# Optimization experiments

Hardware: AMD Instinct MI355X
Metric: run time of the kernel (lower is better)

## Reference

```python
import jax, jax.numpy as jnp
import numpy as np

HIDDEN = 512
INPUT = 512
BATCH = 16384


def _quant_dequant(w):
    # mirrors torch: scale = max(|w|)/127 + 1e-8; int8 round-clamp; dequantize
    scale = jnp.max(jnp.abs(w)) / 127.0 + 1e-8
    q = jnp.clip(jnp.round(w / scale), -128, 127)
    return q * scale


def setup_inputs() -> dict:
    key = jax.random.key(0)
    ks = jax.random.split(key, 7)
    x = jax.random.normal(ks[0], (BATCH, INPUT), dtype=jnp.float32)
    h_prev = jax.random.normal(ks[1], (BATCH, HIDDEN), dtype=jnp.float32)
    c_prev = jax.random.normal(ks[2], (BATCH, HIDDEN), dtype=jnp.float32)
    w_ih = _quant_dequant(jax.random.normal(ks[3], (4 * HIDDEN, INPUT), dtype=jnp.float32) * 0.05)
    w_hh = _quant_dequant(jax.random.normal(ks[4], (4 * HIDDEN, HIDDEN), dtype=jnp.float32) * 0.05)
    bias_ih = jax.random.normal(ks[5], (4 * HIDDEN,), dtype=jnp.float32) * 0.05
    bias_hh = jax.random.normal(ks[6], (4 * HIDDEN,), dtype=jnp.float32) * 0.05
    return {"x": x, "h_prev": h_prev, "c_prev": c_prev,
            "w_ih": w_ih, "w_hh": w_hh, "bias_ih": bias_ih, "bias_hh": bias_hh}


def reference(x, h_prev, c_prev, w_ih, w_hh, bias_ih, bias_hh):
    # gates: [B, 4H]
    gates = x @ w_ih.T + bias_ih + h_prev @ w_hh.T + bias_hh
    i_g, f_g, g_g, o_g = jnp.split(gates, 4, axis=1)
    i_g = jax.nn.sigmoid(i_g)
    f_g = jax.nn.sigmoid(f_g)
    g_g = jnp.tanh(g_g)
    o_g = jax.nn.sigmoid(o_g)
    c_new = f_g * c_prev + i_g * g_g
    h_new = o_g * jnp.tanh(c_new)
    return (h_new, c_new)
```

## Files before the change

### kernel.cpp

```cpp
#include <hip/hip_runtime.h>


typedef __attribute__((ext_vector_type(4))) int int4v;
typedef __attribute__((ext_vector_type(8))) short short8;
typedef __attribute__((ext_vector_type(4))) float f32x4;
typedef unsigned int u32;
typedef unsigned short u16;
typedef unsigned char u8;

#define BATCH 16384
#define HID 512
#define KTOT 1024
#define BM 256
#define KSTEPS 8
#define TILEA_BYTES 32768
#define TILEW_BYTES 16384
#define NBM 64
#define NBN 16
#define WSA_BYTES ((size_t)NBM * KSTEPS * TILEA_BYTES)
#define WSW_BYTES ((size_t)NBN * KSTEPS * TILEW_BYTES)
#define SCALE_OFF (WSA_BYTES + WSW_BYTES)
#define PART_OFF (SCALE_OFF + 65536)
#define SW_OFF (PART_OFF + 2048)
#define WS_NEEDED (SW_OFF + 64)

__device__ __forceinline__ float sigmoidf_(float v) { return 1.0f / (1.0f + __expf(-v)); }
__device__ __forceinline__ float tanhf_(float v) { return 1.0f - 2.0f / (__expf(2.0f * v) + 1.0f); }

__device__ __forceinline__ void gload_lds16(const void* g, void* l) {
    __builtin_amdgcn_global_load_lds(
        (const __attribute__((address_space(1))) u32*)g,
        (__attribute__((address_space(3))) u32*)l, 16, 0, 0);
}

__device__ __forceinline__ u32 pack4(float a, float b, float c, float d, float inv) {
    int q0 = (int)rintf(a * inv), q1 = (int)rintf(b * inv);
    int q2 = (int)rintf(c * inv), q3 = (int)rintf(d * inv);
    return (q0 & 255) | ((q1 & 255) << 8) | ((q2 & 255) << 16) | ((q3 & 255) << 24);
}

__global__ __launch_bounds__(256) void wmax_part(
    const float* __restrict__ w_ih, const float* __restrict__ w_hh, float* __restrict__ part)
{
    const u32 b = blockIdx.x;
    const float* src = (b < 256) ? (w_ih + (size_t)b * 4096) : (w_hh + (size_t)(b - 256) * 4096);
    const u32 t = threadIdx.x;
    float am = 0.f;
    const float4* p = (const float4*)src + t;
    #pragma unroll
    for (int j = 0; j < 4; ++j) {
        float4 v = p[j * 256];
        am = fmaxf(am, fmaxf(fmaxf(fabsf(v.x), fabsf(v.y)), fmaxf(fabsf(v.z), fabsf(v.w))));
    }
    #pragma unroll
    for (int o = 32; o >= 1; o >>= 1) am = fmaxf(am, __shfl_xor(am, o, 64));
    __shared__ float red[4];
    if ((t & 63) == 0) red[t >> 6] = am;
    __syncthreads();
    if (t == 0) part[b] = fmaxf(fmaxf(red[0], red[1]), fmaxf(red[2], red[3]));
}

__global__ __launch_bounds__(256) void pack_w(
    const float* __restrict__ w_ih, const float* __restrict__ w_hh,
    const float* __restrict__ part, u8* __restrict__ wsW, float* __restrict__ swOut)
{
    const u32 t = threadIdx.x;
    float am = fmaxf(part[t], part[t + 256]);
    #pragma unroll
    for (int o = 32; o >= 1; o >>= 1) am = fmaxf(am, __shfl_xor(am, o, 64));
    __shared__ float red[4];
    if ((t & 63) == 0) red[t >> 6] = am;
    __syncthreads();
    const float wmax = fmaxf(fmaxf(red[0], red[1]), fmaxf(red[2], red[3]));
    const float inv = 127.0f / wmax;
    if (blockIdx.x == 0 && t == 0) *swOut = wmax * (1.0f / 127.0f);

    const u32 widx = blockIdx.x * 256 + t;
    const u32 cphys = widx & 7;
    const u32 row = (widx >> 3) & 127;
    const u32 ks = (widx >> 10) & 7;
    const u32 bn = widx >> 13;
    const u32 clog = cphys ^ (row & 7);
    const u32 g = row >> 5, rr = row & 31;
    const u32 wrow = g * 512 + bn * 32 + rr;
    const u32 kglob = ks * 128 + clog * 16;
    const float* src = (kglob < 512) ? (w_ih + (size_t)wrow * 512 + kglob)
                                     : (w_hh + (size_t)wrow * 512 + (kglob - 512));
    u32 wds[4];
    #pragma unroll
    for (int j = 0; j < 4; ++j) {
        float4 v = *((const float4*)src + j);
        wds[j] = pack4(v.x, v.y, v.z, v.w, inv);
    }
    int4v val = {(int)wds[0], (int)wds[1], (int)wds[2], (int)wds[3]};
    *(int4v*)(wsW + (size_t)widx * 16) = val;
}

__global__ __launch_bounds__(256) void pack_a(
    const float* __restrict__ x, const float* __restrict__ h_prev,
    u8* __restrict__ wsA, float* __restrict__ aScale)
{
    const u32 t = threadIdx.x;
    const u32 lane = t & 63;
    const u32 m = blockIdx.x * 4 + (t >> 6);
    const u32 k0 = lane * 16;
    const float* src = (k0 < 512) ? (x + (size_t)m * 512 + k0)
                                  : (h_prev + (size_t)m * 512 + (k0 - 512));
    float4 v[4];
    #pragma unroll
    for (int j = 0; j < 4; ++j) v[j] = *((const float4*)src + j);
    float am = 0.f;
    #pragma unroll
    for (int j = 0; j < 4; ++j)
        am = fmaxf(am, fmaxf(fmaxf(fabsf(v[j].x), fabsf(v[j].y)),
                             fmaxf(fabsf(v[j].z), fabsf(v[j].w))));
    #pragma unroll
    for (int o = 32; o >= 1; o >>= 1) am = fmaxf(am, __shfl_xor(am, o, 64));
    const float inv = (am > 0.f) ? 127.0f / am : 0.f;
    if (lane == 0) aScale[m] = am * (1.0f / 127.0f);
    u32 wds[4];
    #pragma unroll
    for (int j = 0; j < 4; ++j) wds[j] = pack4(v[j].x, v[j].y, v[j].z, v[j].w, inv);
    const u32 bm = m >> 8, row = m & 255;
    const u32 ks = lane >> 3, clog = lane & 7;
    const u32 cphys = clog ^ (row & 7);
    int4v val = {(int)wds[0], (int)wds[1], (int)wds[2], (int)wds[3]};
    *(int4v*)(wsA + ((((size_t)bm * 8 + ks) * 256 + row) * 8 + cphys) * 16) = val;
}

__global__ __launch_bounds__(256, 2) void lstm_gemm(
    const u8* __restrict__ wsA, const u8* __restrict__ wsW,
    const float* __restrict__ aScale, const float* __restrict__ swPtr,
    const float* __restrict__ c_prev,
    const float* __restrict__ b_ih, const float* __restrict__ b_hh,
    float* __restrict__ h_out, float* __restrict__ c_out)
{
    __shared__ u8 sA[TILEA_BYTES];
    __shared__ u8 sW[TILEW_BYTES];

    const int t = threadIdx.x;
    const int bn = blockIdx.x & 15;
    const int bm = blockIdx.x >> 4;
    const int n0 = bn * 32;
    const int rowBase = bm * BM;

    const int lane = t & 63;
    const int wv = t >> 6;
    const int colin = lane & 15;
    const int quad = lane >> 4;
    const int stageOff = t * 16;

    int4v acc[4][2][4];
    #pragma unroll
    for (int rf = 0; rf < 4; ++rf)
        #pragma unroll
        for (int cc = 0; cc < 2; ++cc)
            #pragma unroll
            for (int g = 0; g < 4; ++g)
                acc[rf][cc][g] = (int4v){0, 0, 0, 0};

    const char* gA = (const char*)wsA + (size_t)bm * KSTEPS * TILEA_BYTES;
    const char* gW = (const char*)wsW + (size_t)bn * KSTEPS * TILEW_BYTES;

    #pragma unroll 1
    for (int ks = 0; ks < KSTEPS; ++ks) {
        __syncthreads();
        #pragma unroll
        for (int j = 0; j < 8; ++j)
            gload_lds16(gA + (size_t)ks * TILEA_BYTES + j * 4096 + stageOff,
                        (char*)sA + j * 4096 + stageOff);
        #pragma unroll
        for (int j = 0; j < 4; ++j)
            gload_lds16(gW + (size_t)ks * TILEW_BYTES + j * 4096 + stageOff,
                        (char*)sW + j * 4096 + stageOff);
        __syncthreads();

        #pragma unroll
        for (int ks2 = 0; ks2 < 2; ++ks2) {
            int4v af[4];
            #pragma unroll
            for (int rf = 0; rf < 4; ++rf) {
                const int row = wv * 64 + rf * 16 + colin;
                const int boff = row * 128 + (((ks2 * 4 + quad) ^ (row & 7)) * 16);
                af[rf] = *(const int4v*)((const char*)sA + boff);
            }
            int4v bfr[2][4];
            #pragma unroll
            for (int cc = 0; cc < 2; ++cc)
                #pragma unroll
                for (int g = 0; g < 4; ++g) {
                    const int wrow = g * 32 + cc * 16 + colin;
                    const int boff = wrow * 128 + (((ks2 * 4 + quad) ^ (wrow & 7)) * 16);
                    bfr[cc][g] = *(const int4v*)((const char*)sW + boff);
                }
            #pragma unroll
            for (int rf = 0; rf < 4; ++rf)
                #pragma unroll
                for (int cc = 0; cc < 2; ++cc)
                    #pragma unroll
                    for (int g = 0; g < 4; ++g)
                        acc[rf][cc][g] = __builtin_amdgcn_mfma_i32_16x16x64_i8(
                            af[rf], bfr[cc][g], acc[rf][cc][g], 0, 0, 0);
        }
    }

    const float sw = *swPtr;
    float rsc[4][4];
    #pragma unroll
    for (int rf = 0; rf < 4; ++rf)
        #pragma unroll
        for (int reg = 0; reg < 4; ++reg)
            rsc[rf][reg] = aScale[rowBase + wv * 64 + rf * 16 + quad * 4 + reg] * sw;

    float bsum[2][4];
    #pragma unroll
    for (int cc = 0; cc < 2; ++cc) {
        const int colg = n0 + cc * 16 + colin;
        #pragma unroll
        for (int g = 0; g < 4; ++g)
            bsum[cc][g] = b_ih[g * 512 + colg] + b_hh[g * 512 + colg];
    }

    #pragma unroll
    for (int rf = 0; rf < 4; ++rf)
        #pragma unroll
        for (int cc = 0; cc < 2; ++cc) {
            const int colg = n0 + cc * 16 + colin;
            #pragma unroll
            for (int reg = 0; reg < 4; ++reg) {
                const int row = rowBase + wv * 64 + rf * 16 + quad * 4 + reg;
                const size_t off = (size_t)row * 512 + colg;
                const float s = rsc[rf][reg];
                const float ig = (float)acc[rf][cc][0][reg] * s + bsum[cc][0];
                const float fg = (float)acc[rf][cc][1][reg] * s + bsum[cc][1];
                const float gg = (float)acc[rf][cc][2][reg] * s + bsum[cc][2];
                const float og = (float)acc[rf][cc][3][reg] * s + bsum[cc][3];
                const float cp = __builtin_nontemporal_load(c_prev + off);
                const float cn = sigmoidf_(fg) * cp + sigmoidf_(ig) * tanhf_(gg);
                const float hn = sigmoidf_(og) * tanhf_(cn);
                __builtin_nontemporal_store(hn, h_out + off);
                __builtin_nontemporal_store(cn, c_out + off);
            }
        }
}

#define LDSK 72
__device__ __forceinline__ u16 f2bf(float f) {
    u32 u = __builtin_bit_cast(u32, f);
    u += 0x7FFFu + ((u >> 16) & 1u);
    return (u16)(u >> 16);
}
__global__ __launch_bounds__(256, 3) void lstm_fused_v1(
    const float* __restrict__ x, const float* __restrict__ h_prev,
    const float* __restrict__ c_prev, const float* __restrict__ w_ih,
    const float* __restrict__ w_hh, const float* __restrict__ b_ih,
    const float* __restrict__ b_hh, float* __restrict__ h_out,
    float* __restrict__ c_out)
{
    __shared__ u16 sA[128][LDSK];
    __shared__ u16 sW[128][LDSK];
    const int t = threadIdx.x;
    const int bn = blockIdx.x & 15, bm = blockIdx.x >> 4;
    const int n0 = bn * 32, rowBase = bm * 128;
    const int srow = t >> 4, scol = t & 15;
    const int lane = t & 63, wv = t >> 6, colin = lane & 15, quad = lane >> 4;
    f32x4 acc[2][2][4];
    #pragma unroll
    for (int rf = 0; rf < 2; ++rf)
        #pragma unroll
        for (int cc = 0; cc < 2; ++cc)
            #pragma unroll
            for (int g = 0; g < 4; ++g) acc[rf][cc][g] = (f32x4){0.f, 0.f, 0.f, 0.f};
    for (int k0 = 0; k0 < KTOT; k0 += 64) {
        const int kk = (k0 < 512) ? k0 : (k0 - 512);
        const float* aSrc = (k0 < 512) ? x : h_prev;
        const float* wSrc = (k0 < 512) ? w_ih : w_hh;
        __syncthreads();
        #pragma unroll
        for (int p = 0; p < 8; ++p) {
            const int r = srow + p * 16;
            const float4 av = *(const float4*)(aSrc + (size_t)(rowBase + r) * 512 + kk + scol * 4);
            ushort4 ap; ap.x = f2bf(av.x); ap.y = f2bf(av.y); ap.z = f2bf(av.z); ap.w = f2bf(av.w);
            *(ushort4*)&sA[r][scol * 4] = ap;
            const int gate = r >> 5, rr = r & 31;
            const float4 wvv = *(const float4*)(wSrc + (size_t)(gate * 512 + n0 + rr) * 512 + kk + scol * 4);
            ushort4 wp; wp.x = f2bf(wvv.x); wp.y = f2bf(wvv.y); wp.z = f2bf(wvv.z); wp.w = f2bf(wvv.w);
            *(ushort4*)&sW[r][scol * 4] = wp;
        }
        __syncthreads();
        #pragma unroll
        for (int ks = 0; ks < 2; ++ks) {
            short8 af[2];
            #pragma unroll
            for (int rf = 0; rf < 2; ++rf)
                af[rf] = *(const short8*)&sA[wv * 32 + rf * 16 + colin][ks * 32 + quad * 8];
            short8 bfr[2][4];
            #pragma unroll
            for (int cc = 0; cc < 2; ++cc)
                #pragma unroll
                for (int g = 0; g < 4; ++g)
                    bfr[cc][g] = *(const short8*)&sW[g * 32 + cc * 16 + colin][ks * 32 + quad * 8];
            #pragma unroll
            for (int rf = 0; rf < 2; ++rf)
                #pragma unroll
                for (int cc = 0; cc < 2; ++cc)
                    #pragma unroll
                    for (int g = 0; g < 4; ++g)
                        acc[rf][cc][g] = __builtin_amdgcn_mfma_f32_16x16x32_bf16(
                            af[rf], bfr[cc][g], acc[rf][cc][g], 0, 0, 0);
        }
    }
    float bsum[2][4];
    #pragma unroll
    for (int cc = 0; cc < 2; ++cc) {
        const int colg = n0 + cc * 16 + colin;
        #pragma unroll
        for (int g = 0; g < 4; ++g) bsum[cc][g] = b_ih[g * 512 + colg] + b_hh[g * 512 + colg];
    }
    #pragma unroll
    for (int rf = 0; rf < 2; ++rf)
        #pragma unroll
        for (int cc = 0; cc < 2; ++cc) {
            const int colg = n0 + cc * 16 + colin;
            #pragma unroll
            for (int reg = 0; reg < 4; ++reg) {
                const int row = rowBase + wv * 32 + rf * 16 + quad * 4 + reg;
                const size_t off = (size_t)row * 512 + colg;
                const float ig = acc[rf][cc][0][reg] + bsum[cc][0];
                const float fg = acc[rf][cc][1][reg] + bsum[cc][1];
                const float gg = acc[rf][cc][2][reg] + bsum[cc][2];
                const float og = acc[rf][cc][3][reg] + bsum[cc][3];
                const float cp = c_prev[off];
                const float cn = sigmoidf_(fg) * cp + sigmoidf_(ig) * tanhf_(gg);
                const float hn = sigmoidf_(og) * tanhf_(cn);
                h_out[off] = hn;
                c_out[off] = cn;
            }
        }
}

extern "C" void kernel_launch(void* const* d_in, const int* in_sizes, int n_in,
                              void* d_out, int out_size, void* d_ws, size_t ws_size,
                              hipStream_t stream) {
    const float* x      = (const float*)d_in[0];
    const float* h_prev = (const float*)d_in[1];
    const float* c_prev = (const float*)d_in[2];
    const float* w_ih   = (const float*)d_in[3];
    const float* w_hh   = (const float*)d_in[4];
    const float* b_ih   = (const float*)d_in[5];
    const float* b_hh   = (const float*)d_in[6];
    float* h_out = (float*)d_out;
    float* c_out = h_out + (size_t)BATCH * HID;

    if (ws_size >= WS_NEEDED) {
        u8* wsA = (u8*)d_ws;
        u8* wsW = (u8*)d_ws + WSA_BYTES;
        float* aScale = (float*)((char*)d_ws + SCALE_OFF);
        float* part   = (float*)((char*)d_ws + PART_OFF);
        float* swOut  = (float*)((char*)d_ws + SW_OFF);
        wmax_part<<<512, 256, 0, stream>>>(w_ih, w_hh, part);
        pack_w<<<512, 256, 0, stream>>>(w_ih, w_hh, part, wsW, swOut);
        pack_a<<<BATCH / 4, 256, 0, stream>>>(x, h_prev, wsA, aScale);
        lstm_gemm<<<NBM * NBN, 256, 0, stream>>>(wsA, wsW, aScale, swOut, c_prev,
                                                 b_ih, b_hh, h_out, c_out);
    } else {
        lstm_fused_v1<<<128 * 16, 256, 0, stream>>>(x, h_prev, c_prev, w_ih, w_hh,
                                                    b_ih, b_hh, h_out, c_out);
    }
}
```

Measured before the change: 214.3 us.

## Load A fragments directly to registers and double-buffer W tiles in LDS

The activation quantization kernel now writes A in an MFMA-fragment-ordered layout, so each GEMM wave can fetch its A operands straight from global memory into registers instead of staging them through LDS. The W tile is double-buffered in LDS, and the next k-step's A and W are prefetched while the current step computes, with one barrier per step instead of two. This removes LDS traffic and synchronization for A and overlaps loads with MFMA work. In exchange it holds two sets of A fragments in registers, which may raise register pressure and lower occupancy; with the K loop fully unrolled and 256 accumulator registers already live, spills are possible.

```diff
diff --git a/kernel.cpp b/kernel.cpp
--- a/kernel.cpp
+++ b/kernel.cpp
@@ -121,11 +121,19 @@
     u32 wds[4];
     #pragma unroll
     for (int j = 0; j < 4; ++j) wds[j] = pack4(v[j].x, v[j].y, v[j].z, v[j].w, inv);
-    const u32 bm = m >> 8, row = m & 255;
-    const u32 ks = lane >> 3, clog = lane & 7;
-    const u32 cphys = clog ^ (row & 7);
+
+    const u32 bm = m >> 8;
+    const u32 row = m & 255;
+    const u32 wv = row >> 6;
+    const u32 rf = (row >> 4) & 3;
+    const u32 colin = row & 15;
+    const u32 ks = lane >> 3;
+    const u32 cit = lane & 7;
+    const u32 ks2 = cit >> 2, quad = cit & 3;
+    const u32 c = rf * 2 + ks2;
     int4v val = {(int)wds[0], (int)wds[1], (int)wds[2], (int)wds[3]};
-    *(int4v*)(wsA + ((((size_t)bm * 8 + ks) * 256 + row) * 8 + cphys) * 16) = val;
+    *(int4v*)(wsA + ((((size_t)bm * 8 + ks) * 4 + wv) * 8 + c) * 1024
+                    + (quad * 16 + colin) * 16) = val;
 }
 
 __global__ __launch_bounds__(256, 2) void lstm_gemm(
@@ -135,8 +143,7 @@
     const float* __restrict__ b_ih, const float* __restrict__ b_hh,
     float* __restrict__ h_out, float* __restrict__ c_out)
 {
-    __shared__ u8 sA[TILEA_BYTES];
-    __shared__ u8 sW[TILEW_BYTES];
+    __shared__ u8 sW[2][TILEW_BYTES];
 
     const int t = threadIdx.x;
     const int bn = blockIdx.x & 15;
@@ -159,31 +166,33 @@
             for (int g = 0; g < 4; ++g)
                 acc[rf][cc][g] = (int4v){0, 0, 0, 0};
 
-    const char* gA = (const char*)wsA + (size_t)bm * KSTEPS * TILEA_BYTES;
-    const char* gW = (const char*)wsW + (size_t)bn * KSTEPS * TILEW_BYTES;
-
-    #pragma unroll 1
+    const char* gA = (const char*)wsA + (size_t)bm * (KSTEPS * TILEA_BYTES)
+                     + wv * 8192 + lane * 16;
+    const char* gW = (const char*)wsW + (size_t)bn * (KSTEPS * TILEW_BYTES);
+
+    int4v areg[2][8];
+    #pragma unroll
+    for (int c = 0; c < 8; ++c)
+        areg[0][c] = *(const int4v*)(gA + c * 1024);
+    #pragma unroll
+    for (int j = 0; j < 4; ++j)
+        gload_lds16(gW + j * 4096 + stageOff, &sW[0][0] + j * 4096 + stageOff);
+    __syncthreads();
+
+    #pragma unroll
     for (int ks = 0; ks < KSTEPS; ++ks) {
-        __syncthreads();
-        #pragma unroll
-        for (int j = 0; j < 8; ++j)
-            gload_lds16(gA + (size_t)ks * TILEA_BYTES + j * 4096 + stageOff,
-                        (char*)sA + j * 4096 + stageOff);
-        #pragma unroll
-        for (int j = 0; j < 4; ++j)
-            gload_lds16(gW + (size_t)ks * TILEW_BYTES + j * 4096 + stageOff,
-                        (char*)sW + j * 4096 + stageOff);
-        __syncthreads();
-
+        const int cur = ks & 1, nxt = cur ^ 1;
+        if (ks < KSTEPS - 1) {
+            #pragma unroll
+            for (int j = 0; j < 4; ++j)
+                gload_lds16(gW + (size_t)(ks + 1) * TILEW_BYTES + j * 4096 + stageOff,
+                            &sW[nxt][0] + j * 4096 + stageOff);
+            #pragma unroll
+            for (int c = 0; c < 8; ++c)
+                areg[nxt][c] = *(const int4v*)(gA + (size_t)(ks + 1) * TILEA_BYTES + c * 1024);
+        }
         #pragma unroll
         for (int ks2 = 0; ks2 < 2; ++ks2) {
-            int4v af[4];
-            #pragma unroll
-            for (int rf = 0; rf < 4; ++rf) {
-                const int row = wv * 64 + rf * 16 + colin;
-                const int boff = row * 128 + (((ks2 * 4 + quad) ^ (row & 7)) * 16);
-                af[rf] = *(const int4v*)((const char*)sA + boff);
-            }
             int4v bfr[2][4];
             #pragma unroll
             for (int cc = 0; cc < 2; ++cc)
@@ -191,7 +200,7 @@
                 for (int g = 0; g < 4; ++g) {
                     const int wrow = g * 32 + cc * 16 + colin;
                     const int boff = wrow * 128 + (((ks2 * 4 + quad) ^ (wrow & 7)) * 16);
-                    bfr[cc][g] = *(const int4v*)((const char*)sW + boff);
+                    bfr[cc][g] = *(const int4v*)(&sW[cur][0] + boff);
                 }
             #pragma unroll
             for (int rf = 0; rf < 4; ++rf)
@@ -200,8 +209,9 @@
                     #pragma unroll
                     for (int g = 0; g < 4; ++g)
                         acc[rf][cc][g] = __builtin_amdgcn_mfma_i32_16x16x64_i8(
-                            af[rf], bfr[cc][g], acc[rf][cc][g], 0, 0, 0);
-        }
+                            areg[cur][rf * 2 + ks2], bfr[cc][g], acc[rf][cc][g], 0, 0, 0);
+        }
+        if (ks < KSTEPS - 1) __syncthreads();
     }
 
     const float sw = *swPtr;
```

Result: slower. 231.8 us (+8.2%).
